# Performance work log

Hardware: AMD Instinct MI355X
Metric: run time of the kernel (lower is better)

The kernel has to match this reference:

```python
import jax, jax.numpy as jnp
import numpy as np

B, D, C, E, H = 65536, 512, 101, 8, 256


def setup_inputs() -> dict:
    key = jax.random.key(0)
    ks = jax.random.split(key, 7)
    s_d = 1.0 / np.sqrt(D)
    s_h = 1.0 / np.sqrt(H)
    return {
        "x": jax.random.normal(ks[0], (B, D), dtype=jnp.float32),
        "W1": jax.random.uniform(ks[1], (E, D, H), jnp.float32, -s_d, s_d),  # expert layer1
        "b1": jax.random.uniform(ks[2], (E, H), jnp.float32, -s_d, s_d),
        "W2": jax.random.uniform(ks[3], (E, H, C), jnp.float32, -s_h, s_h),  # expert layer2
        "b2": jax.random.uniform(ks[4], (E, C), jnp.float32, -s_h, s_h),
        "Wg": jax.random.uniform(ks[5], (D, E), jnp.float32, -s_d, s_d),     # gate
        "bg": jax.random.uniform(ks[6], (E,), jnp.float32, -s_d, s_d),
    }


def reference(x, W1, b1, W2, b2, Wg, bg):
    # gate: softmax over experts
    gates = jax.nn.softmax(x @ Wg + bg, axis=1)                 # [B, E]
    # all experts: batched two-layer MLP
    h = jax.nn.relu(jnp.einsum("bd,edh->beh", x, W1) + b1)      # [B, E, H]
    eo = jnp.einsum("beh,ehc->bec", h, W2) + b2                 # [B, E, C]
    # gate-weighted sum over experts
    return jnp.einsum("be,bec->bc", gates, eo)                  # [B, C]
```

## Files before the change

kernel.cpp:

```cpp
#include <hip/hip_runtime.h>


typedef __attribute__((ext_vector_type(8))) short short8x;
typedef __attribute__((ext_vector_type(4))) float float4x;

#define C_DIM 101

__device__ __forceinline__ unsigned short f2bf(float f) {
  unsigned int u = __builtin_bit_cast(unsigned int, f);
  u += 0x7fffu + ((u >> 16) & 1u);
  return (unsigned short)(u >> 16);
}

__global__ void conv_weights(const float* __restrict__ W1, const float* __restrict__ Wg,
                             const float* __restrict__ W2,
                             unsigned short* __restrict__ W1bf,
                             unsigned short* __restrict__ W2bf) {
  if (blockIdx.x < 516) {
    int s = blockIdx.x * blockDim.x + threadIdx.x;
    int l = s & 63;
    int frag = s >> 6;
    int kf = frag & 15;
    int ntile = frag >> 4;
    int n = (ntile << 4) | (l & 15);
    int k = (kf << 5) | ((l >> 4) << 3);
    short8x v;
#pragma unroll
    for (int j = 0; j < 8; ++j) {
      int kk = k + j;
      float f;
      if (n < 2048)      f = W1[((size_t)(n >> 8) * 512 + kk) * 256 + (n & 255)];
      else if (n < 2056) f = Wg[(size_t)kk * 8 + (n - 2048)];
      else               f = 0.f;
      v[j] = (short)f2bf(f);
    }
    *(short8x*)(W1bf + (size_t)s * 8) = v;
  } else {
    int s = (blockIdx.x - 516) * blockDim.x + threadIdx.x;
    int l = s & 63;
    int frag = s >> 6;
    int kf = frag & 63;
    int ntile = frag >> 6;
    int c = (ntile << 4) | (l & 15);
    int k = (kf << 5) | ((l >> 4) << 3);
    short8x v;
#pragma unroll
    for (int j = 0; j < 8; ++j) {
      int kk = k + j;
      float f = (c < C_DIM) ? W2[((size_t)(kk >> 8) * 256 + (kk & 255)) * C_DIM + c] : 0.f;
      v[j] = (short)f2bf(f);
    }
    *(short8x*)(W2bf + (size_t)s * 8) = v;
  }
}

__global__ __launch_bounds__(512, 2) void moe_main(
    const float* __restrict__ x, const float* __restrict__ b1,
    const float* __restrict__ b2, const float* __restrict__ bg,
    const unsigned short* __restrict__ W1bf, const unsigned short* __restrict__ W2bf,
    float* __restrict__ out) {
  __shared__ unsigned short xA[64 * 512];
  __shared__ unsigned short hA[64 * 512];
  __shared__ float gt[8 * 64];
  float* graw = (float*)hA;

  const int tid = threadIdx.x;
  const int w = tid >> 6;
  const int l = tid & 63;
  const int quad = l >> 4;
  const int p = l & 15;
  const int r0 = blockIdx.x * 64;

#pragma unroll
  for (int it = 0; it < 8; ++it) {
    int g = tid + it * 512;
    int m = g >> 6;
    int k0 = (g & 63) << 3;
    const float* src = x + (size_t)(r0 + m) * 512 + k0;
    float4 f0 = *(const float4*)src;
    float4 f1 = *(const float4*)(src + 4);
    short8x v;
    v[0] = (short)f2bf(f0.x); v[1] = (short)f2bf(f0.y);
    v[2] = (short)f2bf(f0.z); v[3] = (short)f2bf(f0.w);
    v[4] = (short)f2bf(f1.x); v[5] = (short)f2bf(f1.y);
    v[6] = (short)f2bf(f1.z); v[7] = (short)f2bf(f1.w);
    int mt = m >> 4;
    int kfrag = k0 >> 5;
    int lane = (((k0 >> 3) & 3) << 4) | (m & 15);
    *(short8x*)&xA[(size_t)(((mt << 4) | kfrag) * 64 + lane) * 8] = v;
  }
  __syncthreads();

  if (w < 4) {
    float4x acc = {0.f, 0.f, 0.f, 0.f};
#pragma unroll 2
    for (int kf = 0; kf < 16; ++kf) {
      short8x a = *(const short8x*)&xA[(size_t)((w * 16 + kf) * 64 + l) * 8];
      short8x b = *(const short8x*)(W1bf + ((size_t)(128 * 16 + kf) * 512 + l * 8));
      acc = __builtin_amdgcn_mfma_f32_16x16x32_bf16(a, b, acc, 0, 0, 0);
    }
    if (p < 8) {
      float bgv = bg[p];
#pragma unroll
      for (int r = 0; r < 4; ++r)
        graw[(w * 16 + quad * 4 + r) * 8 + p] = acc[r] + bgv;
    }
  }
  __syncthreads();
  if (tid < 64) {
    float v[8], mx = -1e30f;
#pragma unroll
    for (int e = 0; e < 8; ++e) { v[e] = graw[tid * 8 + e]; mx = fmaxf(mx, v[e]); }
    float s = 0.f;
#pragma unroll
    for (int e = 0; e < 8; ++e) { v[e] = expf(v[e] - mx); s += v[e]; }
    float inv = 1.f / s;
#pragma unroll
    for (int e = 0; e < 8; ++e) gt[e * 64 + tid] = v[e] * inv;
  }
  __syncthreads();

  float4x zero = {0.f, 0.f, 0.f, 0.f};
  float4x acc2[4];
  acc2[0] = zero; acc2[1] = zero; acc2[2] = zero; acc2[3] = zero;

  for (int it = 0; it < 4; ++it) {
#pragma unroll
    for (int eo = 0; eo < 2; ++eo) {
      const int e = it * 2 + eo;
      float4x acc1[4][2];
#pragma unroll
      for (int mt = 0; mt < 4; ++mt) { acc1[mt][0] = zero; acc1[mt][1] = zero; }

      const unsigned short* __restrict__ bp =
          W1bf + ((size_t)(e * 16 + w * 2) * 16) * 512 + (size_t)l * 8;
      short8x bA0 = *(const short8x*)(bp);
      short8x bA1 = *(const short8x*)(bp + 8192);
      short8x bB0, bB1;
#pragma unroll
      for (int kf = 0; kf < 16; kf += 2) {
        bB0 = *(const short8x*)(bp + (kf + 1) * 512);
        bB1 = *(const short8x*)(bp + 8192 + (kf + 1) * 512);
#pragma unroll
        for (int mt = 0; mt < 4; ++mt) {
          short8x a = *(const short8x*)&xA[(size_t)((mt * 16 + kf) * 64 + l) * 8];
          acc1[mt][0] = __builtin_amdgcn_mfma_f32_16x16x32_bf16(a, bA0, acc1[mt][0], 0, 0, 0);
          acc1[mt][1] = __builtin_amdgcn_mfma_f32_16x16x32_bf16(a, bA1, acc1[mt][1], 0, 0, 0);
        }
        if (kf + 2 < 16) {
          bA0 = *(const short8x*)(bp + (kf + 2) * 512);
          bA1 = *(const short8x*)(bp + 8192 + (kf + 2) * 512);
        }
#pragma unroll
        for (int mt = 0; mt < 4; ++mt) {
          short8x a = *(const short8x*)&xA[(size_t)((mt * 16 + kf + 1) * 64 + l) * 8];
          acc1[mt][0] = __builtin_amdgcn_mfma_f32_16x16x32_bf16(a, bB0, acc1[mt][0], 0, 0, 0);
          acc1[mt][1] = __builtin_amdgcn_mfma_f32_16x16x32_bf16(a, bB1, acc1[mt][1], 0, 0, 0);
        }
      }

      if (eo == 0) __syncthreads();

      float4x gv0 = *(const float4x*)&gt[e * 64 + 0  + quad * 4];
      float4x gv1 = *(const float4x*)&gt[e * 64 + 16 + quad * 4];
      float4x gv2 = *(const float4x*)&gt[e * 64 + 32 + quad * 4];
      float4x gv3 = *(const float4x*)&gt[e * 64 + 48 + quad * 4];
#pragma unroll
      for (int nc = 0; nc < 2; ++nc) {
        int cw = w * 32 + nc * 16 + p;
        float b1v = b1[e * 256 + cw];
        int jj = p & 7;
        int ldbase = ((nc * 2 + (p >> 3)) << 4);
#pragma unroll
        for (int mt = 0; mt < 4; ++mt) {
          float4x gv = (mt == 0) ? gv0 : (mt == 1) ? gv1 : (mt == 2) ? gv2 : gv3;
#pragma unroll
          for (int r = 0; r < 4; ++r) {
            float hv = fmaxf(acc1[mt][nc][r] + b1v, 0.f) * gv[r];
            hA[(size_t)((eo * 32 + w * 4 + mt) * 512) + (ldbase + quad * 4 + r) * 8 + jj] =
                f2bf(hv);
          }
        }
      }
    }
    __syncthreads();

    if (w < 7) {
      const unsigned short* __restrict__ bp2 =
          W2bf + ((size_t)(w * 64 + it * 16)) * 512 + (size_t)l * 8;
#pragma unroll
      for (int eo = 0; eo < 2; ++eo) {
#pragma unroll
        for (int kf2 = 0; kf2 < 8; ++kf2) {
          short8x b = *(const short8x*)(bp2 + (size_t)(eo * 8 + kf2) * 512);
#pragma unroll
          for (int mt = 0; mt < 4; ++mt) {
            short8x a = *(const short8x*)&hA[(size_t)((eo * 32 + kf2 * 4 + mt) * 64 + l) * 8];
            acc2[mt] = __builtin_amdgcn_mfma_f32_16x16x32_bf16(a, b, acc2[mt], 0, 0, 0);
          }
        }
      }
    }
  }

  if (w < 7) {
    int c = w * 16 + p;
    if (c < C_DIM) {
#pragma unroll
      for (int mt = 0; mt < 4; ++mt) {
#pragma unroll
        for (int r = 0; r < 4; ++r) {
          int row = mt * 16 + quad * 4 + r;
          float bias = 0.f;
#pragma unroll
          for (int e = 0; e < 8; ++e) bias += gt[e * 64 + row] * b2[e * C_DIM + c];
          out[(size_t)(r0 + row) * C_DIM + c] = acc2[mt][r] + bias;
        }
      }
    }
  }
}

extern "C" void kernel_launch(void* const* d_in, const int* in_sizes, int n_in,
                              void* d_out, int out_size, void* d_ws, size_t ws_size,
                              hipStream_t stream) {
  const float* x  = (const float*)d_in[0];
  const float* W1 = (const float*)d_in[1];
  const float* b1 = (const float*)d_in[2];
  const float* W2 = (const float*)d_in[3];
  const float* b2 = (const float*)d_in[4];
  const float* Wg = (const float*)d_in[5];
  const float* bg = (const float*)d_in[6];
  float* out = (float*)d_out;

  unsigned short* W1bf = (unsigned short*)d_ws;
  unsigned short* W2bf = (unsigned short*)((char*)d_ws + (size_t)129 * 16 * 512 * 2);

  conv_weights<<<644, 256, 0, stream>>>(W1, Wg, W2, W1bf, W2bf);
  moe_main<<<1024, 512, 0, stream>>>(x, b1, b2, bg, W1bf, W2bf, out);
}
```

Before: 399.3 us.

## Retile expert GEMMs across warps for 2x4 layer-1 and balanced layer-2 work

Layer 1 now gives each warp 2 row tiles by 4 column tiles (rows split in halves, columns in quarters) instead of 4x2. Each warp therefore loads fewer shared-memory A fragments per B fragment. Layer 2 now spreads work over all 8 warps, each owning one row tile and up to 4 output column tiles, instead of leaving one warp idle and having each warp cover all rows. The trade-off is more global W2 fragment loads per warp in layer 2 and four live B registers in layer 1, which raises register pressure.

```diff
diff --git a/kernel.cpp b/kernel.cpp
--- a/kernel.cpp
+++ b/kernel.cpp
@@ -70,6 +70,10 @@
   const int quad = l >> 4;
   const int p = l & 15;
   const int r0 = blockIdx.x * 64;
+  const int rh = w >> 2;
+  const int cq = w & 3;
+  const int mt_own = w >> 1;
+  const int cg = w & 1;
 
 #pragma unroll
   for (int it = 0; it < 8; ++it) {
@@ -128,94 +132,99 @@
 #pragma unroll
     for (int eo = 0; eo < 2; ++eo) {
       const int e = it * 2 + eo;
-      float4x acc1[4][2];
-#pragma unroll
-      for (int mt = 0; mt < 4; ++mt) { acc1[mt][0] = zero; acc1[mt][1] = zero; }
+      float4x acc1[2][4];
+#pragma unroll
+      for (int mtl = 0; mtl < 2; ++mtl)
+#pragma unroll
+        for (int nc = 0; nc < 4; ++nc) acc1[mtl][nc] = zero;
 
       const unsigned short* __restrict__ bp =
-          W1bf + ((size_t)(e * 16 + w * 2) * 16) * 512 + (size_t)l * 8;
-      short8x bA0 = *(const short8x*)(bp);
-      short8x bA1 = *(const short8x*)(bp + 8192);
-      short8x bB0, bB1;
+          W1bf + ((size_t)(e * 16 + cq * 4) * 16) * 512 + (size_t)l * 8;
+      short8x bA[4], bB[4];
+#pragma unroll
+      for (int nc = 0; nc < 4; ++nc) bA[nc] = *(const short8x*)(bp + nc * 8192);
+
 #pragma unroll
       for (int kf = 0; kf < 16; kf += 2) {
-        bB0 = *(const short8x*)(bp + (kf + 1) * 512);
-        bB1 = *(const short8x*)(bp + 8192 + (kf + 1) * 512);
-#pragma unroll
-        for (int mt = 0; mt < 4; ++mt) {
-          short8x a = *(const short8x*)&xA[(size_t)((mt * 16 + kf) * 64 + l) * 8];
-          acc1[mt][0] = __builtin_amdgcn_mfma_f32_16x16x32_bf16(a, bA0, acc1[mt][0], 0, 0, 0);
-          acc1[mt][1] = __builtin_amdgcn_mfma_f32_16x16x32_bf16(a, bA1, acc1[mt][1], 0, 0, 0);
+#pragma unroll
+        for (int nc = 0; nc < 4; ++nc)
+          bB[nc] = *(const short8x*)(bp + nc * 8192 + (kf + 1) * 512);
+        short8x a0 = *(const short8x*)&xA[(size_t)(((rh * 2 + 0) * 16 + kf) * 64 + l) * 8];
+        short8x a1 = *(const short8x*)&xA[(size_t)(((rh * 2 + 1) * 16 + kf) * 64 + l) * 8];
+#pragma unroll
+        for (int nc = 0; nc < 4; ++nc) {
+          acc1[0][nc] = __builtin_amdgcn_mfma_f32_16x16x32_bf16(a0, bA[nc], acc1[0][nc], 0, 0, 0);
+          acc1[1][nc] = __builtin_amdgcn_mfma_f32_16x16x32_bf16(a1, bA[nc], acc1[1][nc], 0, 0, 0);
         }
         if (kf + 2 < 16) {
-          bA0 = *(const short8x*)(bp + (kf + 2) * 512);
-          bA1 = *(const short8x*)(bp + 8192 + (kf + 2) * 512);
-        }
-#pragma unroll
-        for (int mt = 0; mt < 4; ++mt) {
-          short8x a = *(const short8x*)&xA[(size_t)((mt * 16 + kf + 1) * 64 + l) * 8];
-          acc1[mt][0] = __builtin_amdgcn_mfma_f32_16x16x32_bf16(a, bB0, acc1[mt][0], 0, 0, 0);
-          acc1[mt][1] = __builtin_amdgcn_mfma_f32_16x16x32_bf16(a, bB1, acc1[mt][1], 0, 0, 0);
+#pragma unroll
+          for (int nc = 0; nc < 4; ++nc)
+            bA[nc] = *(const short8x*)(bp + nc * 8192 + (kf + 2) * 512);
+        }
+        short8x a2 = *(const short8x*)&xA[(size_t)(((rh * 2 + 0) * 16 + kf + 1) * 64 + l) * 8];
+        short8x a3 = *(const short8x*)&xA[(size_t)(((rh * 2 + 1) * 16 + kf + 1) * 64 + l) * 8];
+#pragma unroll
+        for (int nc = 0; nc < 4; ++nc) {
+          acc1[0][nc] = __builtin_amdgcn_mfma_f32_16x16x32_bf16(a2, bB[nc], acc1[0][nc], 0, 0, 0);
+          acc1[1][nc] = __builtin_amdgcn_mfma_f32_16x16x32_bf16(a3, bB[nc], acc1[1][nc], 0, 0, 0);
         }
       }
 
       if (eo == 0) __syncthreads();
 
-      float4x gv0 = *(const float4x*)&gt[e * 64 + 0  + quad * 4];
-      float4x gv1 = *(const float4x*)&gt[e * 64 + 16 + quad * 4];
-      float4x gv2 = *(const float4x*)&gt[e * 64 + 32 + quad * 4];
-      float4x gv3 = *(const float4x*)&gt[e * 64 + 48 + quad * 4];
-#pragma unroll
-      for (int nc = 0; nc < 2; ++nc) {
-        int cw = w * 32 + nc * 16 + p;
+      float4x gv0 = *(const float4x*)&gt[e * 64 + rh * 32 + 0  + quad * 4];
+      float4x gv1 = *(const float4x*)&gt[e * 64 + rh * 32 + 16 + quad * 4];
+#pragma unroll
+      for (int nc = 0; nc < 4; ++nc) {
+        int cw = cq * 64 + nc * 16 + p;
         float b1v = b1[e * 256 + cw];
-        int jj = p & 7;
-        int ldbase = ((nc * 2 + (p >> 3)) << 4);
-#pragma unroll
-        for (int mt = 0; mt < 4; ++mt) {
-          float4x gv = (mt == 0) ? gv0 : (mt == 1) ? gv1 : (mt == 2) ? gv2 : gv3;
+        int kf2g = cw >> 5;
+        int koff = cw & 31;
+        int jj = koff & 7;
+        int ldbase = (koff >> 3) << 4;
+#pragma unroll
+        for (int mtl = 0; mtl < 2; ++mtl) {
+          int frag = eo * 32 + kf2g * 4 + (rh * 2 + mtl);
+          float4x gv = mtl ? gv1 : gv0;
 #pragma unroll
           for (int r = 0; r < 4; ++r) {
-            float hv = fmaxf(acc1[mt][nc][r] + b1v, 0.f) * gv[r];
-            hA[(size_t)((eo * 32 + w * 4 + mt) * 512) + (ldbase + quad * 4 + r) * 8 + jj] =
-                f2bf(hv);
+            float hv = fmaxf(acc1[mtl][nc][r] + b1v, 0.f) * gv[r];
+            hA[(size_t)frag * 512 + (ldbase + quad * 4 + r) * 8 + jj] = f2bf(hv);
           }
         }
       }
     }
     __syncthreads();
 
-    if (w < 7) {
-      const unsigned short* __restrict__ bp2 =
-          W2bf + ((size_t)(w * 64 + it * 16)) * 512 + (size_t)l * 8;
-#pragma unroll
-      for (int eo = 0; eo < 2; ++eo) {
-#pragma unroll
-        for (int kf2 = 0; kf2 < 8; ++kf2) {
-          short8x b = *(const short8x*)(bp2 + (size_t)(eo * 8 + kf2) * 512);
-#pragma unroll
-          for (int mt = 0; mt < 4; ++mt) {
-            short8x a = *(const short8x*)&hA[(size_t)((eo * 32 + kf2 * 4 + mt) * 64 + l) * 8];
-            acc2[mt] = __builtin_amdgcn_mfma_f32_16x16x32_bf16(a, b, acc2[mt], 0, 0, 0);
+#pragma unroll
+    for (int eo = 0; eo < 2; ++eo) {
+#pragma unroll
+      for (int kf2 = 0; kf2 < 8; ++kf2) {
+        short8x a = *(const short8x*)&hA[(size_t)((eo * 32 + kf2 * 4 + mt_own) * 64 + l) * 8];
+#pragma unroll
+        for (int ct2 = 0; ct2 < 4; ++ct2) {
+          int ct = cg * 4 + ct2;
+          if (ct < 7) {
+            short8x b = *(const short8x*)(W2bf +
+                ((size_t)(ct * 64 + it * 16 + eo * 8 + kf2)) * 512 + (size_t)l * 8);
+            acc2[ct2] = __builtin_amdgcn_mfma_f32_16x16x32_bf16(a, b, acc2[ct2], 0, 0, 0);
           }
         }
       }
     }
   }
 
-  if (w < 7) {
-    int c = w * 16 + p;
+#pragma unroll
+  for (int ct2 = 0; ct2 < 4; ++ct2) {
+    int c = (cg * 4 + ct2) * 16 + p;
     if (c < C_DIM) {
 #pragma unroll
-      for (int mt = 0; mt < 4; ++mt) {
-#pragma unroll
-        for (int r = 0; r < 4; ++r) {
-          int row = mt * 16 + quad * 4 + r;
-          float bias = 0.f;
-#pragma unroll
-          for (int e = 0; e < 8; ++e) bias += gt[e * 64 + row] * b2[e * C_DIM + c];
-          out[(size_t)(r0 + row) * C_DIM + c] = acc2[mt][r] + bias;
-        }
+      for (int r = 0; r < 4; ++r) {
+        int row = mt_own * 16 + quad * 4 + r;
+        float bias = 0.f;
+#pragma unroll
+        for (int e = 0; e < 8; ++e) bias += gt[e * 64 + row] * b2[e * C_DIM + c];
+        out[(size_t)(r0 + row) * C_DIM + c] = acc2[ct2][r] + bias;
       }
     }
   }
```

Result: slower. 584.4 us (+46.3%).

## Split second GEMM by K per wave and reduce partial outputs through LDS

Applied to the files above, without the earlier changes.

Each wave now consumes its own slice of the hidden activations for the second GEMM right after producing them, keeping a private per-wave hA buffer and accumulating all 7 output column tiles in registers. This removes the block-wide barriers inside the expert loop and the shared hA round trip across waves. The 8 waves' partial sums are then reduced through LDS, reusing the xA buffer, before the bias and store. In exchange, per-thread accumulators grow from 4 to 28 float4 values, which raises register pressure at launch_bounds(512,2), and a reduction phase with extra barriers is added at the end.

```diff
diff --git a/kernel.cpp b/kernel.cpp
--- a/kernel.cpp
+++ b/kernel.cpp
@@ -60,9 +60,10 @@
     const unsigned short* __restrict__ W1bf, const unsigned short* __restrict__ W2bf,
     float* __restrict__ out) {
   __shared__ unsigned short xA[64 * 512];
-  __shared__ unsigned short hA[64 * 512];
+  __shared__ unsigned short hA[8 * 4 * 512];
   __shared__ float gt[8 * 64];
   float* graw = (float*)hA;
+  float* red  = (float*)xA;
 
   const int tid = threadIdx.x;
   const int w = tid >> 6;
@@ -70,6 +71,7 @@
   const int quad = l >> 4;
   const int p = l & 15;
   const int r0 = blockIdx.x * 64;
+  unsigned short* hAw = hA + w * 4 * 512;
 
 #pragma unroll
   for (int it = 0; it < 8; ++it) {
@@ -121,103 +123,110 @@
   __syncthreads();
 
   float4x zero = {0.f, 0.f, 0.f, 0.f};
-  float4x acc2[4];
-  acc2[0] = zero; acc2[1] = zero; acc2[2] = zero; acc2[3] = zero;
-
-  for (int it = 0; it < 4; ++it) {
-#pragma unroll
-    for (int eo = 0; eo < 2; ++eo) {
-      const int e = it * 2 + eo;
-      float4x acc1[4][2];
-#pragma unroll
-      for (int mt = 0; mt < 4; ++mt) { acc1[mt][0] = zero; acc1[mt][1] = zero; }
-
-      const unsigned short* __restrict__ bp =
-          W1bf + ((size_t)(e * 16 + w * 2) * 16) * 512 + (size_t)l * 8;
-      short8x bA0 = *(const short8x*)(bp);
-      short8x bA1 = *(const short8x*)(bp + 8192);
-      short8x bB0, bB1;
-#pragma unroll
-      for (int kf = 0; kf < 16; kf += 2) {
-        bB0 = *(const short8x*)(bp + (kf + 1) * 512);
-        bB1 = *(const short8x*)(bp + 8192 + (kf + 1) * 512);
-#pragma unroll
-        for (int mt = 0; mt < 4; ++mt) {
-          short8x a = *(const short8x*)&xA[(size_t)((mt * 16 + kf) * 64 + l) * 8];
-          acc1[mt][0] = __builtin_amdgcn_mfma_f32_16x16x32_bf16(a, bA0, acc1[mt][0], 0, 0, 0);
-          acc1[mt][1] = __builtin_amdgcn_mfma_f32_16x16x32_bf16(a, bA1, acc1[mt][1], 0, 0, 0);
+  float4x acc2[4][7];
+#pragma unroll
+  for (int mt = 0; mt < 4; ++mt)
+#pragma unroll
+    for (int ct = 0; ct < 7; ++ct) acc2[mt][ct] = zero;
+
+  for (int e = 0; e < 8; ++e) {
+    float4x acc1[4][2];
+#pragma unroll
+    for (int mt = 0; mt < 4; ++mt) { acc1[mt][0] = zero; acc1[mt][1] = zero; }
+
+    const unsigned short* __restrict__ bp =
+        W1bf + ((size_t)(e * 16 + w * 2) * 16) * 512 + (size_t)l * 8;
+    short8x bA0 = *(const short8x*)(bp);
+    short8x bA1 = *(const short8x*)(bp + 8192);
+    short8x bB0, bB1;
+#pragma unroll
+    for (int kf = 0; kf < 16; kf += 2) {
+      bB0 = *(const short8x*)(bp + (kf + 1) * 512);
+      bB1 = *(const short8x*)(bp + 8192 + (kf + 1) * 512);
+#pragma unroll
+      for (int mt = 0; mt < 4; ++mt) {
+        short8x a = *(const short8x*)&xA[(size_t)((mt * 16 + kf) * 64 + l) * 8];
+        acc1[mt][0] = __builtin_amdgcn_mfma_f32_16x16x32_bf16(a, bA0, acc1[mt][0], 0, 0, 0);
+        acc1[mt][1] = __builtin_amdgcn_mfma_f32_16x16x32_bf16(a, bA1, acc1[mt][1], 0, 0, 0);
+      }
+      if (kf + 2 < 16) {
+        bA0 = *(const short8x*)(bp + (kf + 2) * 512);
+        bA1 = *(const short8x*)(bp + 8192 + (kf + 2) * 512);
+      }
+#pragma unroll
+      for (int mt = 0; mt < 4; ++mt) {
+        short8x a = *(const short8x*)&xA[(size_t)((mt * 16 + kf + 1) * 64 + l) * 8];
+        acc1[mt][0] = __builtin_amdgcn_mfma_f32_16x16x32_bf16(a, bB0, acc1[mt][0], 0, 0, 0);
+        acc1[mt][1] = __builtin_amdgcn_mfma_f32_16x16x32_bf16(a, bB1, acc1[mt][1], 0, 0, 0);
+      }
+    }
+
+    float4x gv0 = *(const float4x*)&gt[e * 64 + 0  + quad * 4];
+    float4x gv1 = *(const float4x*)&gt[e * 64 + 16 + quad * 4];
+    float4x gv2 = *(const float4x*)&gt[e * 64 + 32 + quad * 4];
+    float4x gv3 = *(const float4x*)&gt[e * 64 + 48 + quad * 4];
+#pragma unroll
+    for (int nc = 0; nc < 2; ++nc) {
+      int cw = w * 32 + nc * 16 + p;
+      float b1v = b1[e * 256 + cw];
+      int jj = p & 7;
+      int ldbase = ((nc * 2 + (p >> 3)) << 4);
+#pragma unroll
+      for (int mt = 0; mt < 4; ++mt) {
+        float4x gv = (mt == 0) ? gv0 : (mt == 1) ? gv1 : (mt == 2) ? gv2 : gv3;
+#pragma unroll
+        for (int r = 0; r < 4; ++r) {
+          float hv = fmaxf(acc1[mt][nc][r] + b1v, 0.f) * gv[r];
+          hAw[(size_t)mt * 512 + (ldbase + quad * 4 + r) * 8 + jj] = f2bf(hv);
         }
-        if (kf + 2 < 16) {
-          bA0 = *(const short8x*)(bp + (kf + 2) * 512);
-          bA1 = *(const short8x*)(bp + 8192 + (kf + 2) * 512);
-        }
-#pragma unroll
-        for (int mt = 0; mt < 4; ++mt) {
-          short8x a = *(const short8x*)&xA[(size_t)((mt * 16 + kf + 1) * 64 + l) * 8];
-          acc1[mt][0] = __builtin_amdgcn_mfma_f32_16x16x32_bf16(a, bB0, acc1[mt][0], 0, 0, 0);
-          acc1[mt][1] = __builtin_amdgcn_mfma_f32_16x16x32_bf16(a, bB1, acc1[mt][1], 0, 0, 0);
-        }
-      }
-
-      if (eo == 0) __syncthreads();
-
-      float4x gv0 = *(const float4x*)&gt[e * 64 + 0  + quad * 4];
-      float4x gv1 = *(const float4x*)&gt[e * 64 + 16 + quad * 4];
-      float4x gv2 = *(const float4x*)&gt[e * 64 + 32 + quad * 4];
-      float4x gv3 = *(const float4x*)&gt[e * 64 + 48 + quad * 4];
-#pragma unroll
-      for (int nc = 0; nc < 2; ++nc) {
-        int cw = w * 32 + nc * 16 + p;
-        float b1v = b1[e * 256 + cw];
-        int jj = p & 7;
-        int ldbase = ((nc * 2 + (p >> 3)) << 4);
-#pragma unroll
-        for (int mt = 0; mt < 4; ++mt) {
-          float4x gv = (mt == 0) ? gv0 : (mt == 1) ? gv1 : (mt == 2) ? gv2 : gv3;
-#pragma unroll
-          for (int r = 0; r < 4; ++r) {
-            float hv = fmaxf(acc1[mt][nc][r] + b1v, 0.f) * gv[r];
-            hA[(size_t)((eo * 32 + w * 4 + mt) * 512) + (ldbase + quad * 4 + r) * 8 + jj] =
-                f2bf(hv);
-          }
-        }
+      }
+    }
+
+    short8x am0 = *(const short8x*)&hAw[(size_t)0 * 512 + l * 8];
+    short8x am1 = *(const short8x*)&hAw[(size_t)1 * 512 + l * 8];
+    short8x am2 = *(const short8x*)&hAw[(size_t)2 * 512 + l * 8];
+    short8x am3 = *(const short8x*)&hAw[(size_t)3 * 512 + l * 8];
+    const unsigned short* __restrict__ bp2 =
+        W2bf + ((size_t)(e * 8 + w)) * 512 + (size_t)l * 8;
+#pragma unroll
+    for (int ct = 0; ct < 7; ++ct) {
+      short8x b = *(const short8x*)(bp2 + (size_t)ct * 64 * 512);
+      acc2[0][ct] = __builtin_amdgcn_mfma_f32_16x16x32_bf16(am0, b, acc2[0][ct], 0, 0, 0);
+      acc2[1][ct] = __builtin_amdgcn_mfma_f32_16x16x32_bf16(am1, b, acc2[1][ct], 0, 0, 0);
+      acc2[2][ct] = __builtin_amdgcn_mfma_f32_16x16x32_bf16(am2, b, acc2[2][ct], 0, 0, 0);
+      acc2[3][ct] = __builtin_amdgcn_mfma_f32_16x16x32_bf16(am3, b, acc2[3][ct], 0, 0, 0);
+    }
+  }
+
+  __syncthreads();
+#pragma unroll
+  for (int mt = 0; mt < 4; ++mt) {
+#pragma unroll
+    for (int ct = 0; ct < 7; ++ct) {
+      if (ct != w) {
+        int s = w - (w > ct ? 1 : 0);
+        *(float4x*)&red[((ct * 7 + s) * 64 + l) * 4] = acc2[mt][ct];
       }
     }
     __syncthreads();
-
     if (w < 7) {
-      const unsigned short* __restrict__ bp2 =
-          W2bf + ((size_t)(w * 64 + it * 16)) * 512 + (size_t)l * 8;
-#pragma unroll
-      for (int eo = 0; eo < 2; ++eo) {
-#pragma unroll
-        for (int kf2 = 0; kf2 < 8; ++kf2) {
-          short8x b = *(const short8x*)(bp2 + (size_t)(eo * 8 + kf2) * 512);
-#pragma unroll
-          for (int mt = 0; mt < 4; ++mt) {
-            short8x a = *(const short8x*)&hA[(size_t)((eo * 32 + kf2 * 4 + mt) * 64 + l) * 8];
-            acc2[mt] = __builtin_amdgcn_mfma_f32_16x16x32_bf16(a, b, acc2[mt], 0, 0, 0);
-          }
-        }
-      }
-    }
-  }
-
-  if (w < 7) {
-    int c = w * 16 + p;
-    if (c < C_DIM) {
-#pragma unroll
-      for (int mt = 0; mt < 4; ++mt) {
+      float4x sum = acc2[mt][w];
+#pragma unroll
+      for (int s = 0; s < 7; ++s)
+        sum += *(const float4x*)&red[((w * 7 + s) * 64 + l) * 4];
+      int c = w * 16 + p;
+      if (c < C_DIM) {
 #pragma unroll
         for (int r = 0; r < 4; ++r) {
           int row = mt * 16 + quad * 4 + r;
           float bias = 0.f;
 #pragma unroll
           for (int e = 0; e < 8; ++e) bias += gt[e * 64 + row] * b2[e * C_DIM + c];
-          out[(size_t)(r0 + row) * C_DIM + c] = acc2[mt][r] + bias;
+          out[(size_t)(r0 + row) * C_DIM + c] = sum[r] + bias;
         }
       }
     }
+    __syncthreads();
   }
 }
 
```

New measurement: 923.6 us. 2.31x slower.

## Split experts across wave halves with 4x4 MFMA tiles and staggered K order

Applied to the files above, without the earlier changes.

Each group of four waves now computes one expert of the pair. Each wave owns a 64x64 tile (4 row tiles by 4 column tiles) instead of looping over both experts with 64x32 tiles, which raises operand reuse per loaded B fragment. The K-loop start is rotated per wave to spread LDS and global access across banks and addresses, and the MFMA bursts are wrapped in s_setprio. The hA layout mapping is recomputed for the new column ownership. The larger accumulator array (64 floats) raises register pressure under launch_bounds(512,2), and the software prefetch of B fragments from the old loop is dropped.

```diff
diff --git a/kernel.cpp b/kernel.cpp
--- a/kernel.cpp
+++ b/kernel.cpp
@@ -70,6 +70,9 @@
   const int quad = l >> 4;
   const int p = l & 15;
   const int r0 = blockIdx.x * 64;
+  const int eo = w >> 2;
+  const int wq = w & 3;
+  const int st = w * 2;
 
 #pragma unroll
   for (int it = 0; it < 8; ++it) {
@@ -125,61 +128,68 @@
   acc2[0] = zero; acc2[1] = zero; acc2[2] = zero; acc2[3] = zero;
 
   for (int it = 0; it < 4; ++it) {
-#pragma unroll
-    for (int eo = 0; eo < 2; ++eo) {
-      const int e = it * 2 + eo;
-      float4x acc1[4][2];
-#pragma unroll
-      for (int mt = 0; mt < 4; ++mt) { acc1[mt][0] = zero; acc1[mt][1] = zero; }
-
-      const unsigned short* __restrict__ bp =
-          W1bf + ((size_t)(e * 16 + w * 2) * 16) * 512 + (size_t)l * 8;
-      short8x bA0 = *(const short8x*)(bp);
-      short8x bA1 = *(const short8x*)(bp + 8192);
-      short8x bB0, bB1;
-#pragma unroll
-      for (int kf = 0; kf < 16; kf += 2) {
-        bB0 = *(const short8x*)(bp + (kf + 1) * 512);
-        bB1 = *(const short8x*)(bp + 8192 + (kf + 1) * 512);
-#pragma unroll
-        for (int mt = 0; mt < 4; ++mt) {
-          short8x a = *(const short8x*)&xA[(size_t)((mt * 16 + kf) * 64 + l) * 8];
-          acc1[mt][0] = __builtin_amdgcn_mfma_f32_16x16x32_bf16(a, bA0, acc1[mt][0], 0, 0, 0);
-          acc1[mt][1] = __builtin_amdgcn_mfma_f32_16x16x32_bf16(a, bA1, acc1[mt][1], 0, 0, 0);
-        }
-        if (kf + 2 < 16) {
-          bA0 = *(const short8x*)(bp + (kf + 2) * 512);
-          bA1 = *(const short8x*)(bp + 8192 + (kf + 2) * 512);
-        }
-#pragma unroll
-        for (int mt = 0; mt < 4; ++mt) {
-          short8x a = *(const short8x*)&xA[(size_t)((mt * 16 + kf + 1) * 64 + l) * 8];
-          acc1[mt][0] = __builtin_amdgcn_mfma_f32_16x16x32_bf16(a, bB0, acc1[mt][0], 0, 0, 0);
-          acc1[mt][1] = __builtin_amdgcn_mfma_f32_16x16x32_bf16(a, bB1, acc1[mt][1], 0, 0, 0);
-        }
-      }
-
-      if (eo == 0) __syncthreads();
-
-      float4x gv0 = *(const float4x*)&gt[e * 64 + 0  + quad * 4];
-      float4x gv1 = *(const float4x*)&gt[e * 64 + 16 + quad * 4];
-      float4x gv2 = *(const float4x*)&gt[e * 64 + 32 + quad * 4];
-      float4x gv3 = *(const float4x*)&gt[e * 64 + 48 + quad * 4];
-#pragma unroll
-      for (int nc = 0; nc < 2; ++nc) {
-        int cw = w * 32 + nc * 16 + p;
-        float b1v = b1[e * 256 + cw];
-        int jj = p & 7;
-        int ldbase = ((nc * 2 + (p >> 3)) << 4);
-#pragma unroll
-        for (int mt = 0; mt < 4; ++mt) {
-          float4x gv = (mt == 0) ? gv0 : (mt == 1) ? gv1 : (mt == 2) ? gv2 : gv3;
-#pragma unroll
-          for (int r = 0; r < 4; ++r) {
-            float hv = fmaxf(acc1[mt][nc][r] + b1v, 0.f) * gv[r];
-            hA[(size_t)((eo * 32 + w * 4 + mt) * 512) + (ldbase + quad * 4 + r) * 8 + jj] =
-                f2bf(hv);
-          }
+    const int e = it * 2 + eo;
+    float4x acc1[4][4];
+#pragma unroll
+    for (int mt = 0; mt < 4; ++mt)
+#pragma unroll
+      for (int nc = 0; nc < 4; ++nc) acc1[mt][nc] = zero;
+
+    const unsigned short* __restrict__ bp =
+        W1bf + ((size_t)(e * 16 + wq * 4) * 16) * 512 + (size_t)l * 8;
+#pragma unroll
+    for (int i = 0; i < 16; ++i) {
+      const int kf = (i + st) & 15;
+      short8x b0 = *(const short8x*)(bp + (0 * 16 + kf) * 512);
+      short8x b1f = *(const short8x*)(bp + (1 * 16 + kf) * 512);
+      short8x b2f = *(const short8x*)(bp + (2 * 16 + kf) * 512);
+      short8x b3f = *(const short8x*)(bp + (3 * 16 + kf) * 512);
+      short8x a0 = *(const short8x*)&xA[(size_t)((0 * 16 + kf) * 64 + l) * 8];
+      short8x a1 = *(const short8x*)&xA[(size_t)((1 * 16 + kf) * 64 + l) * 8];
+      short8x a2 = *(const short8x*)&xA[(size_t)((2 * 16 + kf) * 64 + l) * 8];
+      short8x a3 = *(const short8x*)&xA[(size_t)((3 * 16 + kf) * 64 + l) * 8];
+      __builtin_amdgcn_s_setprio(1);
+      acc1[0][0] = __builtin_amdgcn_mfma_f32_16x16x32_bf16(a0, b0, acc1[0][0], 0, 0, 0);
+      acc1[1][0] = __builtin_amdgcn_mfma_f32_16x16x32_bf16(a1, b0, acc1[1][0], 0, 0, 0);
+      acc1[2][0] = __builtin_amdgcn_mfma_f32_16x16x32_bf16(a2, b0, acc1[2][0], 0, 0, 0);
+      acc1[3][0] = __builtin_amdgcn_mfma_f32_16x16x32_bf16(a3, b0, acc1[3][0], 0, 0, 0);
+      acc1[0][1] = __builtin_amdgcn_mfma_f32_16x16x32_bf16(a0, b1f, acc1[0][1], 0, 0, 0);
+      acc1[1][1] = __builtin_amdgcn_mfma_f32_16x16x32_bf16(a1, b1f, acc1[1][1], 0, 0, 0);
+      acc1[2][1] = __builtin_amdgcn_mfma_f32_16x16x32_bf16(a2, b1f, acc1[2][1], 0, 0, 0);
+      acc1[3][1] = __builtin_amdgcn_mfma_f32_16x16x32_bf16(a3, b1f, acc1[3][1], 0, 0, 0);
+      acc1[0][2] = __builtin_amdgcn_mfma_f32_16x16x32_bf16(a0, b2f, acc1[0][2], 0, 0, 0);
+      acc1[1][2] = __builtin_amdgcn_mfma_f32_16x16x32_bf16(a1, b2f, acc1[1][2], 0, 0, 0);
+      acc1[2][2] = __builtin_amdgcn_mfma_f32_16x16x32_bf16(a2, b2f, acc1[2][2], 0, 0, 0);
+      acc1[3][2] = __builtin_amdgcn_mfma_f32_16x16x32_bf16(a3, b2f, acc1[3][2], 0, 0, 0);
+      acc1[0][3] = __builtin_amdgcn_mfma_f32_16x16x32_bf16(a0, b3f, acc1[0][3], 0, 0, 0);
+      acc1[1][3] = __builtin_amdgcn_mfma_f32_16x16x32_bf16(a1, b3f, acc1[1][3], 0, 0, 0);
+      acc1[2][3] = __builtin_amdgcn_mfma_f32_16x16x32_bf16(a2, b3f, acc1[2][3], 0, 0, 0);
+      acc1[3][3] = __builtin_amdgcn_mfma_f32_16x16x32_bf16(a3, b3f, acc1[3][3], 0, 0, 0);
+      __builtin_amdgcn_s_setprio(0);
+    }
+
+    __syncthreads();
+
+    float4x gv0 = *(const float4x*)&gt[e * 64 + 0  + quad * 4];
+    float4x gv1 = *(const float4x*)&gt[e * 64 + 16 + quad * 4];
+    float4x gv2 = *(const float4x*)&gt[e * 64 + 32 + quad * 4];
+    float4x gv3 = *(const float4x*)&gt[e * 64 + 48 + quad * 4];
+#pragma unroll
+    for (int nc = 0; nc < 4; ++nc) {
+      int cw = wq * 64 + nc * 16 + p;
+      float b1v = b1[e * 256 + cw];
+      int kf2 = cw >> 5;
+      int koff = cw & 31;
+      int jj = koff & 7;
+      int ldbase = (koff >> 3) << 4;
+#pragma unroll
+      for (int mt = 0; mt < 4; ++mt) {
+        float4x gv = (mt == 0) ? gv0 : (mt == 1) ? gv1 : (mt == 2) ? gv2 : gv3;
+#pragma unroll
+        for (int r = 0; r < 4; ++r) {
+          float hv = fmaxf(acc1[mt][nc][r] + b1v, 0.f) * gv[r];
+          hA[(size_t)((eo * 32 + kf2 * 4 + mt) * 512) + (ldbase + quad * 4 + r) * 8 + jj] =
+              f2bf(hv);
         }
       }
     }
@@ -189,16 +199,19 @@
       const unsigned short* __restrict__ bp2 =
           W2bf + ((size_t)(w * 64 + it * 16)) * 512 + (size_t)l * 8;
 #pragma unroll
-      for (int eo = 0; eo < 2; ++eo) {
-#pragma unroll
-        for (int kf2 = 0; kf2 < 8; ++kf2) {
-          short8x b = *(const short8x*)(bp2 + (size_t)(eo * 8 + kf2) * 512);
-#pragma unroll
-          for (int mt = 0; mt < 4; ++mt) {
-            short8x a = *(const short8x*)&hA[(size_t)((eo * 32 + kf2 * 4 + mt) * 64 + l) * 8];
-            acc2[mt] = __builtin_amdgcn_mfma_f32_16x16x32_bf16(a, b, acc2[mt], 0, 0, 0);
-          }
-        }
+      for (int i = 0; i < 16; ++i) {
+        const int s = (i + st) & 15;
+        short8x b = *(const short8x*)(bp2 + (size_t)s * 512);
+        short8x a0 = *(const short8x*)&hA[(size_t)((s * 4 + 0) * 64 + l) * 8];
+        short8x a1 = *(const short8x*)&hA[(size_t)((s * 4 + 1) * 64 + l) * 8];
+        short8x a2 = *(const short8x*)&hA[(size_t)((s * 4 + 2) * 64 + l) * 8];
+        short8x a3 = *(const short8x*)&hA[(size_t)((s * 4 + 3) * 64 + l) * 8];
+        __builtin_amdgcn_s_setprio(1);
+        acc2[0] = __builtin_amdgcn_mfma_f32_16x16x32_bf16(a0, b, acc2[0], 0, 0, 0);
+        acc2[1] = __builtin_amdgcn_mfma_f32_16x16x32_bf16(a1, b, acc2[1], 0, 0, 0);
+        acc2[2] = __builtin_amdgcn_mfma_f32_16x16x32_bf16(a2, b, acc2[2], 0, 0, 0);
+        acc2[3] = __builtin_amdgcn_mfma_f32_16x16x32_bf16(a3, b, acc2[3], 0, 0, 0);
+        __builtin_amdgcn_s_setprio(0);
       }
     }
   }
```

Result: slower. 487.1 us (+22.0%).
